# Kernel tuning notes

Hardware: AMD Instinct MI355X
Metric: run time of the kernel (lower is better)

Reference implementation:

```python
import jax, jax.numpy as jnp
import numpy as np

STRIDE = 4
H, W, A = 208, 336, 3
ANCHOR_SCALE = 8.0
ASPECTS = ((1.0, 1.0), (1.4, 0.7), (0.7, 1.4))  # (aspect_x, aspect_y)
PRE_NMS = 2000
POST_NMS = 1000
IOU_THR = 0.7
BBOX_CLIP = float(np.log(1000.0 / 16.0))


def make_anchors():
    # EfficientDet/SageMakerCV-style anchors at level 2, boxes as (y1, x1, y2, x2)
    base = ANCHOR_SCALE * STRIDE  # 32
    yc = (np.arange(H, dtype=np.float32) + 0.5) * STRIDE
    xc = (np.arange(W, dtype=np.float32) + 0.5) * STRIDE
    yy, xx = np.meshgrid(yc, xc, indexing='ij')  # [H, W]
    per_aspect = []
    for ax, ay in ASPECTS:
        hx, hy = base * ax / 2.0, base * ay / 2.0
        per_aspect.append(np.stack([yy - hy, xx - hx, yy + hy, xx + hx], axis=-1))
    return np.stack(per_aspect, axis=2).reshape(-1, 4).astype(np.float32)  # [H*W*A, 4]


def decode(deltas, anchors):
    # deltas: [B, N, 4] (dy, dx, dh, dw); anchors: [N, 4]; weights (1,1,1,1)
    ah = anchors[:, 2] - anchors[:, 0]
    aw = anchors[:, 3] - anchors[:, 1]
    acy = anchors[:, 0] + 0.5 * ah
    acx = anchors[:, 1] + 0.5 * aw
    dy, dx = deltas[..., 0], deltas[..., 1]
    dh = jnp.clip(deltas[..., 2], -BBOX_CLIP, BBOX_CLIP)
    dw = jnp.clip(deltas[..., 3], -BBOX_CLIP, BBOX_CLIP)
    cy = dy * ah + acy
    cx = dx * aw + acx
    h = jnp.exp(dh) * ah
    w = jnp.exp(dw) * aw
    return jnp.stack([cy - 0.5 * h, cx - 0.5 * w, cy + 0.5 * h, cx + 0.5 * w], axis=-1)


def _iou_one_to_many(box, boxes):
    y1 = jnp.maximum(box[0], boxes[:, 0])
    x1 = jnp.maximum(box[1], boxes[:, 1])
    y2 = jnp.minimum(box[2], boxes[:, 2])
    x2 = jnp.minimum(box[3], boxes[:, 3])
    inter = jnp.maximum(y2 - y1, 0.0) * jnp.maximum(x2 - x1, 0.0)
    a1 = (box[2] - box[0]) * (box[3] - box[1])
    a2 = (boxes[:, 2] - boxes[:, 0]) * (boxes[:, 3] - boxes[:, 1])
    return inter / (a1 + a2 - inter + 1e-8)


def nms_single(boxes, scores):
    # greedy NMS, fixed POST_NMS iterations (jit-friendly)
    def body(i, state):
        sc, kb, ks = state
        j = jnp.argmax(sc)
        b, s = boxes[j], sc[j]
        kb = kb.at[i].set(b)
        ks = ks.at[i].set(s)
        sup = _iou_one_to_many(b, boxes) > IOU_THR  # suppresses j itself (iou=1)
        sc = jnp.where(sup, -1.0, sc)
        return sc, kb, ks

    init = (scores,
            jnp.zeros((POST_NMS, 4), boxes.dtype),
            jnp.zeros((POST_NMS,), scores.dtype))
    _, kb, ks = jax.lax.fori_loop(0, POST_NMS, body, init)
    return kb, ks


def setup_inputs() -> dict:
    key = jax.random.key(0)
    k0, k1, k2 = jax.random.split(key, 3)
    feats = jax.random.normal(k0, (2, H, W, 256), dtype=jnp.float32)
    img_info = jnp.ones((2, 2), jnp.float32) * jnp.array([832.0, 1344.0], jnp.float32)
    w_cls = 0.01 * jax.random.normal(k1, (256, A * 1), dtype=jnp.float32)
    b_cls = jnp.zeros((A * 1,), jnp.float32)
    w_reg = 0.01 * jax.random.normal(k2, (256, A * 4), dtype=jnp.float32)
    b_reg = jnp.zeros((A * 4,), jnp.float32)
    return {"feats": feats, "img_info": img_info, "w_cls": w_cls, "b_cls": b_cls,
            "w_reg": w_reg, "b_reg": b_reg}


def reference(feats, img_info, w_cls, b_cls, w_reg, b_reg):
    B = feats.shape[0]
    # 1x1 convs == channel matmuls
    cls_scores = jnp.einsum('bhwc,co->bhwo', feats, w_cls) + b_cls  # [B,H,W,3]
    bbox_preds = jnp.einsum('bhwc,co->bhwo', feats, w_reg) + b_reg  # [B,H,W,12]

    scores = jax.nn.sigmoid(cls_scores).reshape(B, -1)       # [B, N]
    deltas = bbox_preds.reshape(B, -1, 4)                    # [B, N, 4]
    anchors = jnp.asarray(make_anchors())                    # [N, 4]
    boxes = decode(deltas, anchors)                          # [B, N, 4]

    # clip to image extents
    hmax = img_info[:, 0][:, None]
    wmax = img_info[:, 1][:, None]
    boxes = jnp.stack([
        jnp.clip(boxes[..., 0], 0.0, hmax),
        jnp.clip(boxes[..., 1], 0.0, wmax),
        jnp.clip(boxes[..., 2], 0.0, hmax),
        jnp.clip(boxes[..., 3], 0.0, wmax)], axis=-1)

    # per-image pre-NMS topk
    top_s, idx = jax.lax.top_k(scores, PRE_NMS)              # [B, PRE]
    top_b = jnp.take_along_axis(boxes, idx[..., None], axis=1)  # [B, PRE, 4]

    rois, roi_scores = jax.vmap(nms_single)(top_b, top_s)    # [B, POST, 4], [B, POST]
    return cls_scores, bbox_preds, rois, roi_scores
```

## Files before the change

kernel.cpp:

```cpp
#include <hip/hip_runtime.h>
#include <cstdint>
#include <cstddef>

#define HH 208
#define WW 336
#define NA 3
#define NPER 209664
#define NROWS 139776
#define RPI 69888
#define NB 2
#define PRE_K 2000
#define POST_K 1000
#define CAP 8192
#define MW 32
#define MROWS 2048
#define BBOX_CLIP_F 4.135166556742356f

#define WS_HIST   0
#define WS_HIST2  32768
#define WS_META   65536
#define WS_META24 65544
#define WS_CCNT   65552
#define WS_KEEPW  65568
#define WS_CAND   66080
#define WS_SBOX   197152
#define WS_SSC    261152
#define WS_MASK   277248
#define WS_ZERO_WORDS 16392

__device__ __forceinline__ float sigmoidf_ref(float x) {
  return __fdiv_rn(1.0f, __fadd_rn(1.0f, expf(-x)));
}
__device__ __forceinline__ unsigned int score_u(float logit) {
  float s = sigmoidf_ref(logit);
  return __float_as_uint(s) | 0x80000000u;
}

__device__ __forceinline__ unsigned long long bcast64(unsigned long long v, int l) {
  unsigned int lo = (unsigned int)__builtin_amdgcn_readlane((int)(unsigned int)v, l);
  unsigned int hi = (unsigned int)__builtin_amdgcn_readlane((int)(unsigned int)(v >> 32), l);
  return ((unsigned long long)hi << 32) | lo;
}

__device__ __forceinline__ float4 decode_box(const float* __restrict__ bbox,
                                             int b, unsigned int n,
                                             float hmax, float wmax) {
  unsigned int a = n % 3u;
  unsigned int pix = n / 3u;
  unsigned int y = pix / (unsigned int)WW;
  unsigned int x = pix % (unsigned int)WW;
  float yc = ((float)y + 0.5f) * 4.0f;
  float xc = ((float)x + 0.5f) * 4.0f;
  float hx = (a == 0) ? 16.0f : ((a == 1) ? 22.4f : 11.2f);
  float hy = (a == 0) ? 16.0f : ((a == 1) ? 11.2f : 22.4f);
  float ay1 = __fsub_rn(yc, hy), ax1 = __fsub_rn(xc, hx);
  float ay2 = __fadd_rn(yc, hy), ax2 = __fadd_rn(xc, hx);
  float ah = __fsub_rn(ay2, ay1), aw = __fsub_rn(ax2, ax1);
  float acy = __fadd_rn(ay1, __fmul_rn(0.5f, ah));
  float acx = __fadd_rn(ax1, __fmul_rn(0.5f, aw));
  const float* d = bbox + ((size_t)b * NPER + n) * 4u;
  float dy = d[0], dx = d[1];
  float dh = fminf(fmaxf(d[2], -BBOX_CLIP_F), BBOX_CLIP_F);
  float dw = fminf(fmaxf(d[3], -BBOX_CLIP_F), BBOX_CLIP_F);
  float cy = __fadd_rn(__fmul_rn(dy, ah), acy);
  float cx = __fadd_rn(__fmul_rn(dx, aw), acx);
  float hh = __fmul_rn(expf(dh), ah);
  float wwv = __fmul_rn(expf(dw), aw);
  float y1 = __fsub_rn(cy, __fmul_rn(0.5f, hh));
  float x1 = __fsub_rn(cx, __fmul_rn(0.5f, wwv));
  float y2 = __fadd_rn(cy, __fmul_rn(0.5f, hh));
  float x2 = __fadd_rn(cx, __fmul_rn(0.5f, wwv));
  y1 = fminf(fmaxf(y1, 0.0f), hmax);
  x1 = fminf(fmaxf(x1, 0.0f), wmax);
  y2 = fminf(fmaxf(y2, 0.0f), hmax);
  x2 = fminf(fmaxf(x2, 0.0f), wmax);
  return make_float4(y1, x1, y2, x2);
}

__device__ __forceinline__ float iou_ref(float4 bi, float4 bj) {
  float yA = fmaxf(bi.x, bj.x);
  float xA = fmaxf(bi.y, bj.y);
  float yB = fminf(bi.z, bj.z);
  float xB = fminf(bi.w, bj.w);
  float inter = __fmul_rn(fmaxf(__fsub_rn(yB, yA), 0.0f),
                          fmaxf(__fsub_rn(xB, xA), 0.0f));
  float a1 = __fmul_rn(__fsub_rn(bi.z, bi.x), __fsub_rn(bi.w, bi.y));
  float a2 = __fmul_rn(__fsub_rn(bj.z, bj.x), __fsub_rn(bj.w, bj.y));
  float den = __fadd_rn(__fsub_rn(__fadd_rn(a1, a2), inter), 1e-8f);
  return __fdiv_rn(inter, den);
}

__global__ void k_zero(unsigned int* __restrict__ p, int n) {
  int i = blockIdx.x * blockDim.x + threadIdx.x;
  if (i < n) p[i] = 0u;
}

__global__ __launch_bounds__(256, 3) void k_head(
    const float* __restrict__ feats, const float* __restrict__ w_cls,
    const float* __restrict__ b_cls, const float* __restrict__ w_reg,
    const float* __restrict__ b_reg, float* __restrict__ out_cls,
    float* __restrict__ out_bbox, unsigned int* __restrict__ hist) {
  const int b = blockIdx.y;
  const int lane = threadIdx.x & 63;
  const int wid = blockIdx.x * (blockDim.x >> 6) + (threadIdx.x >> 6);
  const int nw = gridDim.x * (blockDim.x >> 6);
  const int k0 = lane << 2;
  const int l15 = lane & 15;
  const int ol = ((l15 & 1) << 3) | ((l15 & 2) << 1) | ((l15 & 4) >> 1) |
                 ((l15 & 8) >> 3);

  __shared__ unsigned int h[4096];
  __shared__ float wt[16][256];
  for (int i = threadIdx.x; i < 4096; i += blockDim.x) {
    h[i] = 0u;
    const int o = i >> 8, c = i & 255;
    wt[o][c] = (o < 3) ? w_cls[c * 3 + o]
                       : (o < 15 ? w_reg[c * 12 + (o - 3)] : 0.0f);
  }
  __syncthreads();

  float4 w0  = *(const float4*)&wt[ol ^ 0][k0];
  float4 w1  = *(const float4*)&wt[ol ^ 1][k0];
  float4 w2  = *(const float4*)&wt[ol ^ 2][k0];
  float4 w3  = *(const float4*)&wt[ol ^ 3][k0];
  float4 w4  = *(const float4*)&wt[ol ^ 4][k0];
  float4 w5  = *(const float4*)&wt[ol ^ 5][k0];
  float4 w6  = *(const float4*)&wt[ol ^ 6][k0];
  float4 w7  = *(const float4*)&wt[ol ^ 7][k0];
  float4 w8  = *(const float4*)&wt[ol ^ 8][k0];
  float4 w9  = *(const float4*)&wt[ol ^ 9][k0];
  float4 w10 = *(const float4*)&wt[ol ^ 10][k0];
  float4 w11 = *(const float4*)&wt[ol ^ 11][k0];
  float4 w12 = *(const float4*)&wt[ol ^ 12][k0];
  float4 w13 = *(const float4*)&wt[ol ^ 13][k0];
  float4 w14 = *(const float4*)&wt[ol ^ 14][k0];
  float4 w15 = *(const float4*)&wt[ol ^ 15][k0];
  float bias = (ol < 3) ? b_cls[ol] : (ol < 15 ? b_reg[ol - 3] : 0.0f);

#define PIN4(W) asm volatile("" : "+v"(W.x), "+v"(W.y), "+v"(W.z), "+v"(W.w))
  PIN4(w0);  PIN4(w1);  PIN4(w2);  PIN4(w3);
  PIN4(w4);  PIN4(w5);  PIN4(w6);  PIN4(w7);
  PIN4(w8);  PIN4(w9);  PIN4(w10); PIN4(w11);
  PIN4(w12); PIN4(w13); PIN4(w14); PIN4(w15);
#undef PIN4
  asm volatile("" : "+v"(bias));

  for (int rr = wid; rr < RPI; rr += 2 * nw) {
    const int rr1 = rr + nw;
    const int has1 = (rr1 < RPI);
    const int r0 = b * RPI + rr;
    const int r1 = b * RPI + (has1 ? rr1 : rr);
    const float4 f0 = *(const float4*)(feats + (size_t)r0 * 256 + k0);
    const float4 f1 = *(const float4*)(feats + (size_t)r1 * 256 + k0);
    float a0[16], a1[16];
#define STEPJ(J, W)                                                        \
    {                                                                      \
      a0[J] = f0.x * W.x; a0[J] += f0.y * W.y;                             \
      a0[J] += f0.z * W.z; a0[J] += f0.w * W.w;                            \
      a1[J] = f1.x * W.x; a1[J] += f1.y * W.y;                             \
      a1[J] += f1.z * W.z; a1[J] += f1.w * W.w;                            \
    }
    STEPJ(0, w0)   STEPJ(1, w1)   STEPJ(2, w2)   STEPJ(3, w3)
    STEPJ(4, w4)   STEPJ(5, w5)   STEPJ(6, w6)   STEPJ(7, w7)
    STEPJ(8, w8)   STEPJ(9, w9)   STEPJ(10, w10) STEPJ(11, w11)
    STEPJ(12, w12) STEPJ(13, w13) STEPJ(14, w14) STEPJ(15, w15)
#undef STEPJ
#pragma unroll
    for (int s = 0; s < 8; ++s) {
      a0[s] += __shfl_xor(a0[8 + s], 1, 64);
      a1[s] += __shfl_xor(a1[8 + s], 1, 64);
    }
#pragma unroll
    for (int s = 0; s < 4; ++s) {
      a0[s] += __shfl_xor(a0[4 + s], 2, 64);
      a1[s] += __shfl_xor(a1[4 + s], 2, 64);
    }
#pragma unroll
    for (int s = 0; s < 2; ++s) {
      a0[s] += __shfl_xor(a0[2 + s], 4, 64);
      a1[s] += __shfl_xor(a1[2 + s], 4, 64);
    }
    a0[0] += __shfl_xor(a0[1], 8, 64);
    a1[0] += __shfl_xor(a1[1], 8, 64);
    a0[0] += __shfl_xor(a0[0], 16, 64);
    a1[0] += __shfl_xor(a1[0], 16, 64);
    a0[0] += __shfl_xor(a0[0], 32, 64);
    a1[0] += __shfl_xor(a1[0], 32, 64);
    if (lane < 16 && ol < 15) {
      float v0 = a0[0] + bias;
      if (ol < 3) {
        out_cls[(size_t)r0 * 3 + ol] = v0;
        atomicAdd(&h[score_u(v0) >> 20], 1u);
      } else {
        out_bbox[(size_t)r0 * 12 + (ol - 3)] = v0;
      }
      if (has1) {
        float v1 = a1[0] + bias;
        if (ol < 3) {
          out_cls[(size_t)r1 * 3 + ol] = v1;
          atomicAdd(&h[score_u(v1) >> 20], 1u);
        } else {
          out_bbox[(size_t)r1 * 12 + (ol - 3)] = v1;
        }
      }
    }
  }
  __syncthreads();
  for (int i = threadIdx.x; i < 4096; i += blockDim.x)
    if (h[i]) atomicAdd(&hist[b * 4096 + i], h[i]);
}

__global__ __launch_bounds__(1024) void k_thresh(const unsigned int* __restrict__ hist,
                                                 unsigned int* __restrict__ meta_T) {
  const int b = blockIdx.x;
  const int t = threadIdx.x;
  __shared__ unsigned int sums[1024];
  unsigned int hb[4];
  unsigned int s = 0u;
#pragma unroll
  for (int q = 0; q < 4; ++q) {
    int bin = 4095 - (t * 4 + q);
    hb[q] = hist[b * 4096 + bin];
    s += hb[q];
  }
  sums[t] = s;
  __syncthreads();
  for (int off = 1; off < 1024; off <<= 1) {
    unsigned int v = (t >= off) ? sums[t - off] : 0u;
    __syncthreads();
    sums[t] += v;
    __syncthreads();
  }
  unsigned int excl = sums[t] - s;
  if (excl < PRE_K && excl + s >= PRE_K) {
    unsigned int c = excl;
#pragma unroll
    for (int q = 0; q < 4; ++q) {
      c += hb[q];
      if (c >= PRE_K) { meta_T[b] = (unsigned int)(4095 - (t * 4 + q)); break; }
    }
  }
}

__global__ __launch_bounds__(256) void k_hist2(const float* __restrict__ out_cls,
                                               const unsigned int* __restrict__ meta_T,
                                               unsigned int* __restrict__ hist2) {
  const int b = blockIdx.y;
  const unsigned int T = meta_T[b];
  __shared__ unsigned int h[4096];
  for (int i = threadIdx.x; i < 4096; i += blockDim.x) h[i] = 0u;
  __syncthreads();
  for (int i = blockIdx.x * blockDim.x + threadIdx.x; i < NPER;
       i += gridDim.x * blockDim.x) {
    unsigned int u = score_u(out_cls[(size_t)b * NPER + i]);
    if ((u >> 20) == T) atomicAdd(&h[(u >> 8) & 0xFFFu], 1u);
  }
  __syncthreads();
  for (int i = threadIdx.x; i < 4096; i += blockDim.x)
    if (h[i]) atomicAdd(&hist2[b * 4096 + i], h[i]);
}

__global__ __launch_bounds__(1024) void k_thresh2(const unsigned int* __restrict__ hist,
                                                  const unsigned int* __restrict__ hist2,
                                                  const unsigned int* __restrict__ meta_T,
                                                  unsigned int* __restrict__ meta_T24) {
  const int b = blockIdx.x;
  const int t = threadIdx.x;
  const unsigned int T = meta_T[b];
  __shared__ unsigned int sums[1024];
  __shared__ unsigned int c0s;
  unsigned int c0 = 0u;
  for (int i = t; i < 4096; i += 1024)
    if ((unsigned int)i > T) c0 += hist[b * 4096 + i];
  sums[t] = c0;
  __syncthreads();
  for (int off = 512; off > 0; off >>= 1) {
    if (t < off) sums[t] += sums[t + off];
    __syncthreads();
  }
  if (t == 0) c0s = sums[0];
  __syncthreads();
  const unsigned int C0 = c0s;
  __syncthreads();
  unsigned int hb[4];
  unsigned int s = 0u;
#pragma unroll
  for (int q = 0; q < 4; ++q) {
    int bin = 4095 - (t * 4 + q);
    hb[q] = hist2[b * 4096 + bin];
    s += hb[q];
  }
  sums[t] = s;
  __syncthreads();
  for (int off = 1; off < 1024; off <<= 1) {
    unsigned int v = (t >= off) ? sums[t - off] : 0u;
    __syncthreads();
    sums[t] += v;
    __syncthreads();
  }
  unsigned int excl = sums[t] - s;
  if (C0 + excl < PRE_K && C0 + excl + s >= PRE_K) {
    unsigned int c = C0 + excl;
#pragma unroll
    for (int q = 0; q < 4; ++q) {
      c += hb[q];
      if (c >= PRE_K) {
        meta_T24[b] = (T << 12) | (unsigned int)(4095 - (t * 4 + q));
        break;
      }
    }
  }
}

__global__ __launch_bounds__(256) void k_compact(const float* __restrict__ out_cls,
                                                 const unsigned int* __restrict__ meta_T24,
                                                 unsigned int* __restrict__ cand_count,
                                                 unsigned long long* __restrict__ cand) {
  const int b = blockIdx.y;
  const unsigned int T24 = meta_T24[b];
  for (int i = blockIdx.x * blockDim.x + threadIdx.x; i < NPER;
       i += gridDim.x * blockDim.x) {
    unsigned int u = score_u(out_cls[(size_t)b * NPER + i]);
    if ((u >> 8) >= T24) {
      unsigned int pos = atomicAdd(&cand_count[b], 1u);
      if (pos < CAP)
        cand[(size_t)b * CAP + pos] =
            ((unsigned long long)u << 32) | (unsigned int)(~(unsigned int)i);
    }
  }
}

__global__ __launch_bounds__(1024) void k_sort(const unsigned long long* __restrict__ cand,
                                               const unsigned int* __restrict__ cand_count,
                                               const float* __restrict__ out_bbox,
                                               const float* __restrict__ img_info,
                                               float* __restrict__ sboxes,
                                               float* __restrict__ sscores) {
  const int b = blockIdx.x;
  const int t = threadIdx.x;
  __shared__ unsigned long long keys[CAP];
  unsigned int cc = cand_count[b];
  if (cc > CAP) cc = CAP;
  int n = 2048;
  while ((unsigned int)n < cc) n <<= 1;
  for (int i = t; i < n; i += 1024)
    keys[i] = (i < (int)cc) ? cand[(size_t)b * CAP + i] : 0ull;
  __syncthreads();
  for (int k = 2; k <= n; k <<= 1) {
    for (int j = k >> 1; j > 0; j >>= 1) {
      for (int i = t; i < n; i += 1024) {
        int ixj = i ^ j;
        if (ixj > i) {
          unsigned long long a = keys[i], c = keys[ixj];
          bool up = ((i & k) == 0);
          bool sw = up ? (a < c) : (a > c);
          if (sw) { keys[i] = c; keys[ixj] = a; }
        }
      }
      __syncthreads();
    }
  }
  const float hmax = img_info[b * 2 + 0];
  const float wmax = img_info[b * 2 + 1];
  for (int i = t; i < PRE_K; i += 1024) {
    unsigned long long key = keys[i];
    unsigned int u = (unsigned int)(key >> 32);
    unsigned int idx = ~(unsigned int)(key & 0xFFFFFFFFull);
    float sc = __uint_as_float(u & 0x7FFFFFFFu);
    float4 bx = decode_box(out_bbox, b, idx, hmax, wmax);
    ((float4*)sboxes)[(size_t)b * PRE_K + i] = bx;
    sscores[(size_t)b * PRE_K + i] = sc;
  }
}

__global__ __launch_bounds__(64) void k_mask(const float* __restrict__ sboxes,
                                             unsigned long long* __restrict__ mask) {
  const int b = blockIdx.z;
  const int rb = blockIdx.x;
  const int cb = blockIdx.y;
  const int t = threadIdx.x;
  if (cb < rb) {
    int i = rb * 64 + t;
    if (i < PRE_K) mask[((size_t)b * MROWS + i) * MW + cb] = 0ull;
    return;
  }
  __shared__ float4 cbox[64];
  const int col0 = cb * 64;
  {
    int c = col0 + t;
    cbox[t] = (c < PRE_K) ? ((const float4*)sboxes)[(size_t)b * PRE_K + c]
                          : make_float4(0.f, 0.f, 0.f, 0.f);
  }
  __syncthreads();
  const int i = rb * 64 + t;
  if (i >= PRE_K) return;
  float4 bi = ((const float4*)sboxes)[(size_t)b * PRE_K + i];
  unsigned long long bits = 0ull;
#pragma unroll 8
  for (int j = 0; j < 64; ++j) {
    int c = col0 + j;
    if (c > i && c < PRE_K) {
      if (iou_ref(bi, cbox[j]) > 0.7f) bits |= (1ull << j);
    }
  }
  mask[((size_t)b * MROWS + i) * MW + cb] = bits;
}

#define MLOAD(BUF, G)                                                     \
  {                                                                       \
    _Pragma("unroll") for (int _k = 0; _k < 32; ++_k) {                   \
      int _row = (G) * 64 + 2 * _k + psel;                                \
      (BUF)[_k] = (_row < PRE_K) ? M[(size_t)(G) * 2048 + 64 * _k + lane] \
                                 : 0ull;                                  \
    }                                                                     \
  }
#define DLOAD(DST, G)                                                     \
  {                                                                       \
    int _row = (G) * 64 + lane;                                           \
    (DST) = ((G) < 32 && _row < PRE_K) ? M[(size_t)_row * MW + (G)] : 0ull; \
  }
#define GSTEP(G, MCUR, MNEXT, DCUR, DNEXT)                                \
  do {                                                                    \
    MLOAD(MNEXT, (G) + 1);                                                \
    DLOAD(DNEXT, (G) + 1);                                                \
    unsigned long long w = bcast64(remv, (G)) | bcast64(remv, (G) + 32);  \
    unsigned long long alive = ~w;                                        \
    if ((G) == 31) alive &= (1ull << (PRE_K - 31 * 64)) - 1ull;           \
    unsigned long long kept = 0ull;                                       \
    while (alive) {                                                       \
      int j = __builtin_ctzll(alive);                                     \
      unsigned long long bit = 1ull << j;                                 \
      kept |= bit;                                                        \
      unsigned long long dj = bcast64((DCUR), j);                         \
      alive &= ~(dj | bit);                                               \
    }                                                                     \
    int pc = __popcll(kept);                                              \
    if (nk + pc >= POST_K) {                                              \
      int need = POST_K - nk;                                             \
      unsigned long long k2 = kept;                                       \
      for (int _t = 0; _t < need; ++_t) k2 &= k2 - 1;                     \
      kept ^= k2;                \
      if (lane == (G)) mykeep = kept;                                     \
      stop = 1;                                                           \
    } else {                                                              \
      nk += pc;                                                           \
      if (lane == (G)) mykeep = kept;                                     \
      unsigned long long keptv = kept >> psel;                            \
      _Pragma("unroll") for (int _q = 0; _q < 32; ++_q) {                 \
        unsigned long long sel = 0ull - ((keptv >> (2 * _q)) & 1ull);     \
        remv |= (MCUR)[_q] & sel;                                         \
      }                                                                   \
    }                                                                     \
  } while (0)

__global__ __launch_bounds__(64, 1) void k_scan(
    const unsigned long long* __restrict__ mask,
    const float* __restrict__ sboxes,
    const float* __restrict__ sscores,
    float* __restrict__ rois,
    float* __restrict__ rsc) {
  const int b = blockIdx.x;
  const int lane = threadIdx.x;
  const int psel = lane >> 5;
  const unsigned long long* M = mask + (size_t)b * MROWS * MW;

  unsigned long long mbA[32], mbB[32], dA, dB;
  unsigned long long remv = 0ull;
  unsigned long long mykeep = 0ull;
  int nk = 0, stop = 0;

  MLOAD(mbA, 0);
  DLOAD(dA, 0);
  for (int g = 0; g < 32; g += 2) {
    GSTEP(g, mbA, mbB, dA, dB);
    if (stop) break;
    GSTEP(g + 1, mbB, mbA, dB, dA);
    if (stop) break;
  }

  int pc = __popcll(mykeep);
  int pref = pc;
#pragma unroll
  for (int off = 1; off < 64; off <<= 1) {
    int v = __shfl_up(pref, off, 64);
    if (lane >= off) pref += v;
  }
  const int excl = pref - pc;
  const int Ktot = __shfl(pref, 63, 64);
  int rank = excl;
  unsigned long long ww = mykeep;
  while (ww) {
    int j = __builtin_ctzll(ww);
    ww &= ww - 1;
    int row = lane * 64 + j;
    ((float4*)rois)[(size_t)b * POST_K + rank] =
        ((const float4*)sboxes)[(size_t)b * PRE_K + row];
    rsc[(size_t)b * POST_K + rank] = sscores[(size_t)b * PRE_K + row];
    ++rank;
  }
  float4 pad = ((const float4*)sboxes)[(size_t)b * PRE_K + 0];
  for (int i = Ktot + lane; i < POST_K; i += 64) {
    ((float4*)rois)[(size_t)b * POST_K + i] = pad;
    rsc[(size_t)b * POST_K + i] = -1.0f;
  }
}

extern "C" void kernel_launch(void* const* d_in, const int* in_sizes, int n_in,
                              void* d_out, int out_size, void* d_ws, size_t ws_size,
                              hipStream_t stream) {
  const float* feats    = (const float*)d_in[0];
  const float* img_info = (const float*)d_in[1];
  const float* w_cls    = (const float*)d_in[2];
  const float* b_cls    = (const float*)d_in[3];
  const float* w_reg    = (const float*)d_in[4];
  const float* b_reg    = (const float*)d_in[5];

  float* out = (float*)d_out;
  float* out_cls  = out;
  float* out_bbox = out + 419328;
  float* out_rois = out + 2096640;
  float* out_rsc  = out + 2104640;

  char* ws = (char*)d_ws;
  unsigned int* hist        = (unsigned int*)(ws + WS_HIST);
  unsigned int* hist2       = (unsigned int*)(ws + WS_HIST2);
  unsigned int* meta_T      = (unsigned int*)(ws + WS_META);
  unsigned int* meta_T24    = (unsigned int*)(ws + WS_META24);
  unsigned int* cand_count  = (unsigned int*)(ws + WS_CCNT);
  unsigned long long* cand  = (unsigned long long*)(ws + WS_CAND);
  float* sboxes             = (float*)(ws + WS_SBOX);
  float* sscores            = (float*)(ws + WS_SSC);
  unsigned long long* mask  = (unsigned long long*)(ws + WS_MASK);

  k_zero<<<(WS_ZERO_WORDS + 255) / 256, 256, 0, stream>>>((unsigned int*)ws, WS_ZERO_WORDS);
  k_head<<<dim3(512, NB), 256, 0, stream>>>(feats, w_cls, b_cls, w_reg, b_reg,
                                            out_cls, out_bbox, hist);
  k_thresh<<<NB, 1024, 0, stream>>>(hist, meta_T);
  k_hist2<<<dim3(128, NB), 256, 0, stream>>>(out_cls, meta_T, hist2);
  k_thresh2<<<NB, 1024, 0, stream>>>(hist, hist2, meta_T, meta_T24);
  k_compact<<<dim3(128, NB), 256, 0, stream>>>(out_cls, meta_T24, cand_count, cand);
  k_sort<<<NB, 1024, 0, stream>>>(cand, cand_count, out_bbox, img_info, sboxes, sscores);
  k_mask<<<dim3(32, 32, NB), 64, 0, stream>>>(sboxes, mask);
  k_scan<<<NB, 64, 0, stream>>>(mask, sboxes, sscores, out_rois, out_rsc);
}
```

Baseline: 393.6 us.

## Fold threshold selection into hist2/compact kernels and launch only upper-triangle mask blocks

Removes the two single-block threshold kernels. Each consumer block now recomputes the histogram suffix-scan selection redundantly in shared memory, which cuts two launches and their serialization from the pipeline. The IoU mask kernel now launches only the 528 upper-triangle tiles, using a triangular index mapping, instead of 1024 blocks with half of them zero-filling. The scan loader masks out lower-triangle words so it never reads the tiles that are no longer written. The cost is redundant scan work in every block and a floating-point sqrt for the index mapping.

```diff
diff --git a/kernel.cpp b/kernel.cpp
--- a/kernel.cpp
+++ b/kernel.cpp
@@ -40,6 +40,43 @@
   unsigned int lo = (unsigned int)__builtin_amdgcn_readlane((int)(unsigned int)v, l);
   unsigned int hi = (unsigned int)__builtin_amdgcn_readlane((int)(unsigned int)(v >> 32), l);
   return ((unsigned long long)hi << 32) | lo;
+}
+
+__device__ __forceinline__ void suffix_select(const unsigned int* __restrict__ H,
+                                              unsigned int C0in, unsigned int need,
+                                              unsigned int base,
+                                              unsigned int* __restrict__ csum,
+                                              unsigned int* __restrict__ outBin,
+                                              unsigned int* __restrict__ outC0) {
+  const int t = threadIdx.x;
+  unsigned int hb[16];
+  unsigned int s = 0u;
+#pragma unroll
+  for (int q = 0; q < 16; ++q) {
+    hb[q] = H[4095 - (t * 16 + q)];
+    s += hb[q];
+  }
+  csum[t] = s;
+  __syncthreads();
+  for (int off = 1; off < 256; off <<= 1) {
+    unsigned int v = (t >= off) ? csum[t - off] : 0u;
+    __syncthreads();
+    csum[t] += v;
+    __syncthreads();
+  }
+  unsigned int excl = C0in + (csum[t] - s);
+  if (excl < need && excl + s >= need) {
+    unsigned int c = excl;
+#pragma unroll
+    for (int q = 0; q < 16; ++q) {
+      c += hb[q];
+      if (c >= need) {
+        *outBin = base | (unsigned int)(4095 - (t * 16 + q));
+        if (outC0) *outC0 = c - hb[q];
+        break;
+      }
+    }
+  }
 }
 
 __device__ __forceinline__ float4 decode_box(const float* __restrict__ bbox,
@@ -210,46 +247,17 @@
     if (h[i]) atomicAdd(&hist[b * 4096 + i], h[i]);
 }
 
-__global__ __launch_bounds__(1024) void k_thresh(const unsigned int* __restrict__ hist,
-                                                 unsigned int* __restrict__ meta_T) {
-  const int b = blockIdx.x;
-  const int t = threadIdx.x;
-  __shared__ unsigned int sums[1024];
-  unsigned int hb[4];
-  unsigned int s = 0u;
-#pragma unroll
-  for (int q = 0; q < 4; ++q) {
-    int bin = 4095 - (t * 4 + q);
-    hb[q] = hist[b * 4096 + bin];
-    s += hb[q];
-  }
-  sums[t] = s;
-  __syncthreads();
-  for (int off = 1; off < 1024; off <<= 1) {
-    unsigned int v = (t >= off) ? sums[t - off] : 0u;
-    __syncthreads();
-    sums[t] += v;
-    __syncthreads();
-  }
-  unsigned int excl = sums[t] - s;
-  if (excl < PRE_K && excl + s >= PRE_K) {
-    unsigned int c = excl;
-#pragma unroll
-    for (int q = 0; q < 4; ++q) {
-      c += hb[q];
-      if (c >= PRE_K) { meta_T[b] = (unsigned int)(4095 - (t * 4 + q)); break; }
-    }
-  }
-}
-
 __global__ __launch_bounds__(256) void k_hist2(const float* __restrict__ out_cls,
-                                               const unsigned int* __restrict__ meta_T,
+                                               const unsigned int* __restrict__ hist,
                                                unsigned int* __restrict__ hist2) {
   const int b = blockIdx.y;
-  const unsigned int T = meta_T[b];
   __shared__ unsigned int h[4096];
+  __shared__ unsigned int csum[256];
+  __shared__ unsigned int Tsh;
   for (int i = threadIdx.x; i < 4096; i += blockDim.x) h[i] = 0u;
-  __syncthreads();
+  suffix_select(hist + b * 4096, 0u, PRE_K, 0u, csum, &Tsh, nullptr);
+  __syncthreads();
+  const unsigned int T = Tsh;
   for (int i = blockIdx.x * blockDim.x + threadIdx.x; i < NPER;
        i += gridDim.x * blockDim.x) {
     unsigned int u = score_u(out_cls[(size_t)b * NPER + i]);
@@ -260,64 +268,20 @@
     if (h[i]) atomicAdd(&hist2[b * 4096 + i], h[i]);
 }
 
-__global__ __launch_bounds__(1024) void k_thresh2(const unsigned int* __restrict__ hist,
-                                                  const unsigned int* __restrict__ hist2,
-                                                  const unsigned int* __restrict__ meta_T,
-                                                  unsigned int* __restrict__ meta_T24) {
-  const int b = blockIdx.x;
-  const int t = threadIdx.x;
-  const unsigned int T = meta_T[b];
-  __shared__ unsigned int sums[1024];
-  __shared__ unsigned int c0s;
-  unsigned int c0 = 0u;
-  for (int i = t; i < 4096; i += 1024)
-    if ((unsigned int)i > T) c0 += hist[b * 4096 + i];
-  sums[t] = c0;
-  __syncthreads();
-  for (int off = 512; off > 0; off >>= 1) {
-    if (t < off) sums[t] += sums[t + off];
-    __syncthreads();
-  }
-  if (t == 0) c0s = sums[0];
-  __syncthreads();
-  const unsigned int C0 = c0s;
-  __syncthreads();
-  unsigned int hb[4];
-  unsigned int s = 0u;
-#pragma unroll
-  for (int q = 0; q < 4; ++q) {
-    int bin = 4095 - (t * 4 + q);
-    hb[q] = hist2[b * 4096 + bin];
-    s += hb[q];
-  }
-  sums[t] = s;
-  __syncthreads();
-  for (int off = 1; off < 1024; off <<= 1) {
-    unsigned int v = (t >= off) ? sums[t - off] : 0u;
-    __syncthreads();
-    sums[t] += v;
-    __syncthreads();
-  }
-  unsigned int excl = sums[t] - s;
-  if (C0 + excl < PRE_K && C0 + excl + s >= PRE_K) {
-    unsigned int c = C0 + excl;
-#pragma unroll
-    for (int q = 0; q < 4; ++q) {
-      c += hb[q];
-      if (c >= PRE_K) {
-        meta_T24[b] = (T << 12) | (unsigned int)(4095 - (t * 4 + q));
-        break;
-      }
-    }
-  }
-}
-
 __global__ __launch_bounds__(256) void k_compact(const float* __restrict__ out_cls,
-                                                 const unsigned int* __restrict__ meta_T24,
+                                                 const unsigned int* __restrict__ hist,
+                                                 const unsigned int* __restrict__ hist2,
                                                  unsigned int* __restrict__ cand_count,
                                                  unsigned long long* __restrict__ cand) {
   const int b = blockIdx.y;
-  const unsigned int T24 = meta_T24[b];
+  __shared__ unsigned int csum[256];
+  __shared__ unsigned int Tsh, C0sh, T24sh;
+  suffix_select(hist + b * 4096, 0u, PRE_K, 0u, csum, &Tsh, &C0sh);
+  __syncthreads();
+  const unsigned int T = Tsh, C0 = C0sh;
+  suffix_select(hist2 + b * 4096, C0, PRE_K, T << 12, csum, &T24sh, nullptr);
+  __syncthreads();
+  const unsigned int T24 = T24sh;
   for (int i = blockIdx.x * blockDim.x + threadIdx.x; i < NPER;
        i += gridDim.x * blockDim.x) {
     unsigned int u = score_u(out_cls[(size_t)b * NPER + i]);
@@ -376,14 +340,12 @@
 __global__ __launch_bounds__(64) void k_mask(const float* __restrict__ sboxes,
                                              unsigned long long* __restrict__ mask) {
   const int b = blockIdx.z;
-  const int rb = blockIdx.x;
-  const int cb = blockIdx.y;
+  const int p = blockIdx.x;
+  const int q = 527 - p;
+  const int kk = (int)((sqrtf((float)(8 * q + 1)) - 1.0f) * 0.5f);
+  const int rb = 31 - kk;
+  const int cb = 31 - (q - kk * (kk + 1) / 2);
   const int t = threadIdx.x;
-  if (cb < rb) {
-    int i = rb * 64 + t;
-    if (i < PRE_K) mask[((size_t)b * MROWS + i) * MW + cb] = 0ull;
-    return;
-  }
   __shared__ float4 cbox[64];
   const int col0 = cb * 64;
   {
@@ -410,8 +372,9 @@
   {                                                                       \
     _Pragma("unroll") for (int _k = 0; _k < 32; ++_k) {                   \
       int _row = (G) * 64 + 2 * _k + psel;                                \
-      (BUF)[_k] = (_row < PRE_K) ? M[(size_t)(G) * 2048 + 64 * _k + lane] \
-                                 : 0ull;                                  \
+      (BUF)[_k] = (_row < PRE_K && (lane & 31) >= (G))                    \
+                      ? M[(size_t)(G) * 2048 + 64 * _k + lane]            \
+                      : 0ull;                                             \
     }                                                                     \
   }
 #define DLOAD(DST, G)                                                     \
@@ -524,8 +487,6 @@
   char* ws = (char*)d_ws;
   unsigned int* hist        = (unsigned int*)(ws + WS_HIST);
   unsigned int* hist2       = (unsigned int*)(ws + WS_HIST2);
-  unsigned int* meta_T      = (unsigned int*)(ws + WS_META);
-  unsigned int* meta_T24    = (unsigned int*)(ws + WS_META24);
   unsigned int* cand_count  = (unsigned int*)(ws + WS_CCNT);
   unsigned long long* cand  = (unsigned long long*)(ws + WS_CAND);
   float* sboxes             = (float*)(ws + WS_SBOX);
@@ -535,11 +496,10 @@
   k_zero<<<(WS_ZERO_WORDS + 255) / 256, 256, 0, stream>>>((unsigned int*)ws, WS_ZERO_WORDS);
   k_head<<<dim3(512, NB), 256, 0, stream>>>(feats, w_cls, b_cls, w_reg, b_reg,
                                             out_cls, out_bbox, hist);
-  k_thresh<<<NB, 1024, 0, stream>>>(hist, meta_T);
-  k_hist2<<<dim3(128, NB), 256, 0, stream>>>(out_cls, meta_T, hist2);
-  k_thresh2<<<NB, 1024, 0, stream>>>(hist, hist2, meta_T, meta_T24);
-  k_compact<<<dim3(128, NB), 256, 0, stream>>>(out_cls, meta_T24, cand_count, cand);
+  k_hist2<<<dim3(128, NB), 256, 0, stream>>>(out_cls, hist, hist2);
+  k_compact<<<dim3(128, NB), 256, 0, stream>>>(out_cls, hist, hist2,
+                                               cand_count, cand);
   k_sort<<<NB, 1024, 0, stream>>>(cand, cand_count, out_bbox, img_info, sboxes, sscores);
-  k_mask<<<dim3(32, 32, NB), 64, 0, stream>>>(sboxes, mask);
+  k_mask<<<dim3(528, 1, NB), 64, 0, stream>>>(sboxes, mask);
   k_scan<<<NB, 64, 0, stream>>>(mask, sboxes, sscores, out_rois, out_rsc);
 }
```

After: 392.7 us. No clear change (-0.2%).
